# Optimization experiments

Hardware: AMD Instinct MI355X
Metric: run time of the kernel (lower is better)

The kernel has to match this reference:

```python
import jax, jax.numpy as jnp
import numpy as np

WINDOW = 2  # window_size

def _causal_window_conv(x, W, b):
    # x: [B,T,D_in], W: [WINDOW, D_in, D_out], b: [D_out]
    # equivalent to left-padding x by WINDOW-1 zeros and a 'valid' conv
    B, T, _ = x.shape
    xp = jnp.pad(x, ((0, 0), (WINDOW - 1, 0), (0, 0)))  # [B, T+WINDOW-1, D_in]
    out = b
    for k in range(WINDOW):
        out = out + jnp.einsum('btd,de->bte', xp[:, k:k + T], W[k])
    return out  # [B,T,D_out]

def setup_inputs() -> dict:
    key = jax.random.key(0)
    ks = jax.random.split(key, 4)
    B, T, Din, Dout = 8, 4096, 256, 256
    scale = 0.05
    x = jax.random.normal(ks[0], (B, T, Din), dtype=jnp.float32)
    W_z = jax.random.normal(ks[1], (WINDOW, Din, Dout), dtype=jnp.float32) * scale
    W_f = jax.random.normal(ks[2], (WINDOW, Din, Dout), dtype=jnp.float32) * scale
    W_o = jax.random.normal(ks[3], (WINDOW, Din, Dout), dtype=jnp.float32) * scale
    b_z = jnp.zeros((Dout,), dtype=jnp.float32)
    b_f = jnp.zeros((Dout,), dtype=jnp.float32)
    b_o = jnp.zeros((Dout,), dtype=jnp.float32)
    return {"x": x, "W_z": W_z, "W_f": W_f, "W_o": W_o,
            "b_z": b_z, "b_f": b_f, "b_o": b_o}

def reference(x, W_z, W_f, W_o, b_z, b_f, b_o):
    # QRNN with fo-pooling (Bradbury et al. 2016), return_sequences=True
    z = jnp.tanh(_causal_window_conv(x, W_z, b_z))          # [B,T,D]
    f = jax.nn.sigmoid(_causal_window_conv(x, W_f, b_f))    # [B,T,D]
    o = jax.nn.sigmoid(_causal_window_conv(x, W_o, b_o))    # [B,T,D]

    def step(c, zfo):
        z_t, f_t, o_t = zfo
        c = f_t * c + (1.0 - f_t) * z_t   # fo-pooling recurrence
        h = o_t * c
        return c, h

    c0 = jnp.zeros(z.shape[::2], dtype=z.dtype)  # [B,D]
    # time-major for scan
    zfo = (z.transpose(1, 0, 2), f.transpose(1, 0, 2), o.transpose(1, 0, 2))
    _, hs = jax.lax.scan(step, c0, zfo)
    return hs.transpose(1, 0, 2)  # [B,T,D]
```

## Files before the change

kernel.cpp:

```cpp
#include <hip/hip_runtime.h>
#include <hip/hip_bf16.h>
#include <hip/hip_fp16.h>

#define BDIM 8
#define TDIM 4096
#define DDIM 256
#define MDIM (BDIM * TDIM)
#define NCHUNK 256
#define LCHUNK (TDIM / NCHUNK)

typedef _Float16 f16x8 __attribute__((ext_vector_type(8)));
typedef _Float16 f16x4 __attribute__((ext_vector_type(4)));
typedef float f32x4 __attribute__((ext_vector_type(4)));

__device__ __forceinline__ float sigmoid_(float x) {
    return 1.0f / (1.0f + __expf(-x));
}
__device__ __forceinline__ float tanh_(float x) {
    return 2.0f / (1.0f + __expf(-2.0f * x)) - 1.0f;
}

#define GLOAD_LDS16(g, l)                                                    \
    __builtin_amdgcn_global_load_lds(                                        \
        (const __attribute__((address_space(1))) void*)(g),                  \
        (__attribute__((address_space(3))) void*)(l), 16, 0, 0)

__global__ __launch_bounds__(256) void convert_x(const float* __restrict__ x,
                                                 _Float16* __restrict__ xpad) {
    const int tp = blockIdx.x * 4 + (threadIdx.x >> 6);
    const int b = blockIdx.y;
    const int q = threadIdx.x & 63;
    if (tp > TDIM) return;
    float4 v = make_float4(0.f, 0.f, 0.f, 0.f);
    if (tp > 0)
        v = *(const float4*)(x + ((size_t)b * TDIM + tp - 1) * DDIM + q * 4);
    f16x4 h;
    h[0] = (_Float16)v.x; h[1] = (_Float16)v.y;
    h[2] = (_Float16)v.z; h[3] = (_Float16)v.w;
    *(f16x4*)(xpad + ((size_t)b * (TDIM + 1) + tp) * DDIM + q * 4) = h;
}

__global__ __launch_bounds__(256) void convert_w(
    const float* __restrict__ Wz, const float* __restrict__ Wf,
    const float* __restrict__ Wo, _Float16* __restrict__ Wt) {
    const int idx = blockIdx.x * 256 + threadIdx.x;
    const int n = idx & 255;
    const int kin = (idx >> 8) & 255;
    const int w = (idx >> 16) & 1;
    const int g = idx >> 17;
    const float* W = (g == 0) ? Wz : (g == 1) ? Wf : Wo;
    const float v = W[(size_t)w * 65536 + (size_t)kin * 256 + n];
    Wt[((size_t)g * 256 + n) * 512 + w * 256 + kin] = (_Float16)v;
}

__global__ __launch_bounds__(256) void gates_mfma(
    const _Float16* __restrict__ xpad, const _Float16* __restrict__ Wt,
    const float* __restrict__ bz, const float* __restrict__ bfv,
    const float* __restrict__ bo,
    _Float16* __restrict__ zbuf, _Float16* __restrict__ fbuf,
    _Float16* __restrict__ obuf) {
    const int hw = blockIdx.x;
    const int logical = (hw & 7) * 192 + (hw >> 3);
    const int mblk = logical / 6;
    const int rem = logical - mblk * 6;
    const int gate = rem % 3;
    const int nblk = rem / 3;
    const int m0 = mblk * 128;
    const int n0 = nblk * 128;

    const int tid = threadIdx.x;
    const int lane = tid & 63;
    const int wave = tid >> 6;
    const int wr = wave >> 1;
    const int wc = wave & 1;

    __shared__ __align__(16) char smem[65536];

    const int s = wave * 64 + lane;
    const int r1 = s >> 2;
    const int kc = (((s & 3) ^ ((s >> 3) & 3))) * 8;

    const int b = m0 >> 12;
    const int t0 = m0 & (TDIM - 1);

    const _Float16* srcA1 =
        xpad + ((size_t)b * (TDIM + 1) + t0 + r1) * DDIM + kc;
    const _Float16* srcA2 = srcA1 + (size_t)64 * DDIM;
    const _Float16* srcB1 = Wt + ((size_t)gate * 256 + n0 + r1) * 512 + kc;
    const _Float16* srcB2 = srcB1 + (size_t)64 * 512;

#define STAGE_(slot, t)                                                      \
    {                                                                        \
        char* dA = smem + (slot) * 16384 + wave * 1024;                      \
        char* dB = smem + (slot) * 16384 + 8192 + wave * 1024;               \
        GLOAD_LDS16(srcA1 + (t) * 32, dA);                                   \
        GLOAD_LDS16(srcA2 + (t) * 32, dA + 4096);                            \
        GLOAD_LDS16(srcB1 + (t) * 32, dB);                                   \
        GLOAD_LDS16(srcB2 + (t) * 32, dB + 4096);                            \
    }

    f32x4 acc[4][4] = {};
    const int am = lane & 15;
    const int kswz = (((lane >> 4) ^ ((lane >> 1) & 3))) * 8;

    STAGE_(0, 0);
    STAGE_(1, 1);
    STAGE_(2, 2);

#pragma unroll
    for (int it = 0; it < 16; ++it) {
        if (it <= 13)
            asm volatile("s_waitcnt vmcnt(8)" ::: "memory");
        else if (it == 14)
            asm volatile("s_waitcnt vmcnt(4)" ::: "memory");
        else
            asm volatile("s_waitcnt vmcnt(0)" ::: "memory");
        __builtin_amdgcn_s_barrier();
        __builtin_amdgcn_sched_barrier(0);
        if (it < 13) STAGE_((it + 3) & 3, it + 3);
        __builtin_amdgcn_sched_barrier(0);

        const _Float16* Ab = (const _Float16*)(smem + (it & 3) * 16384);
        const _Float16* Bb = (const _Float16*)(smem + (it & 3) * 16384 + 8192);

        f16x8 a[4], bb[4];
#pragma unroll
        for (int i = 0; i < 4; ++i)
            a[i] = *(const f16x8*)(Ab + (wr * 64 + i * 16 + am) * 32 + kswz);
#pragma unroll
        for (int j = 0; j < 4; ++j)
            bb[j] = *(const f16x8*)(Bb + (wc * 64 + j * 16 + am) * 32 + kswz);

        asm volatile("s_waitcnt lgkmcnt(0)" ::: "memory");
        __builtin_amdgcn_sched_barrier(0);
        __builtin_amdgcn_s_setprio(1);
#pragma unroll
        for (int i = 0; i < 4; ++i)
#pragma unroll
            for (int j = 0; j < 4; ++j)
                acc[i][j] = __builtin_amdgcn_mfma_f32_16x16x32_f16(
                    bb[j], a[i], acc[i][j], 0, 0, 0);
        __builtin_amdgcn_s_setprio(0);
        __builtin_amdgcn_sched_barrier(0);
    }
#undef STAGE_

    const float* bias = (gate == 0) ? bz : (gate == 1) ? bfv : bo;
    _Float16* outp = (gate == 0) ? zbuf : (gate == 1) ? fbuf : obuf;
    const int nq = (lane >> 4) * 4;
#pragma unroll
    for (int i = 0; i < 4; ++i) {
        const size_t gm = (size_t)(m0 + wr * 64 + i * 16 + am);
#pragma unroll
        for (int j = 0; j < 4; ++j) {
            const int gc = n0 + wc * 64 + j * 16 + nq;
            const float4 b4 = *(const float4*)(bias + gc);
            f32x4 v = acc[i][j];
            f16x4 h;
            if (gate == 0) {
                h[0] = (_Float16)tanh_(v[0] + b4.x);
                h[1] = (_Float16)tanh_(v[1] + b4.y);
                h[2] = (_Float16)tanh_(v[2] + b4.z);
                h[3] = (_Float16)tanh_(v[3] + b4.w);
            } else {
                h[0] = (_Float16)sigmoid_(v[0] + b4.x);
                h[1] = (_Float16)sigmoid_(v[1] + b4.y);
                h[2] = (_Float16)sigmoid_(v[2] + b4.z);
                h[3] = (_Float16)sigmoid_(v[3] + b4.w);
            }
            *(f16x4*)(outp + gm * DDIM + gc) = h;
        }
    }
}

__global__ __launch_bounds__(256) void scan_pass1(
    const _Float16* __restrict__ zbuf, const _Float16* __restrict__ fbuf,
    float* __restrict__ aggA, float* __restrict__ aggB) {
    const int idx = blockIdx.x * 256 + threadIdx.x;
    const int d4 = idx & 63;
    const int chunk = (idx >> 6) & (NCHUNK - 1);
    const int b = idx >> 14;

    const size_t row0 = (size_t)b * TDIM + (size_t)chunk * LCHUNK;
    const int2* zp = (const int2*)zbuf + row0 * 64 + d4;
    const int2* fp = (const int2*)fbuf + row0 * 64 + d4;

    float A[4], c[4];
#pragma unroll
    for (int e = 0; e < 4; ++e) { A[e] = 1.0f; c[e] = 0.0f; }

    for (int i = 0; i < LCHUNK; ++i) {
        int2 fv = *fp;
        int2 zv = *zp;
        const _Float16* fh = (const _Float16*)&fv;
        const _Float16* zh = (const _Float16*)&zv;
#pragma unroll
        for (int e = 0; e < 4; ++e) {
            const float f = (float)fh[e];
            const float z = (float)zh[e];
            A[e] *= f;
            c[e] = f * c[e] + (1.0f - f) * z;
        }
        fp += 64;
        zp += 64;
    }
    ((float4*)aggA)[idx] = make_float4(A[0], A[1], A[2], A[3]);
    ((float4*)aggB)[idx] = make_float4(c[0], c[1], c[2], c[3]);
}

__global__ __launch_bounds__(256) void carry_scan(
    const float* __restrict__ aggA, const float* __restrict__ aggB,
    float* __restrict__ carry) {
    const int g = blockIdx.x * 256 + threadIdx.x;
    const int d = g & 255;
    const int b = g >> 8;
    const size_t base = (size_t)b * NCHUNK * 256 + d;

    float c = 0.0f;
    for (int ch0 = 0; ch0 < NCHUNK; ch0 += 16) {
        float A[16], Bv[16];
#pragma unroll
        for (int u = 0; u < 16; ++u) {
            const size_t p = base + (size_t)(ch0 + u) * 256;
            A[u] = aggA[p];
            Bv[u] = aggB[p];
        }
#pragma unroll
        for (int u = 0; u < 16; ++u) {
            const size_t p = base + (size_t)(ch0 + u) * 256;
            carry[p] = c;
            c = A[u] * c + Bv[u];
        }
    }
}

__global__ __launch_bounds__(256) void scan_pass2(
    const _Float16* __restrict__ zbuf, const _Float16* __restrict__ fbuf,
    const _Float16* __restrict__ obuf, const float* __restrict__ carry,
    float* __restrict__ out) {
    const int idx = blockIdx.x * 256 + threadIdx.x;
    const int d4 = idx & 63;
    const int chunk = (idx >> 6) & (NCHUNK - 1);
    const int b = idx >> 14;

    float c[4];
    const float4 c0 = ((const float4*)carry)[idx];
    c[0] = c0.x; c[1] = c0.y; c[2] = c0.z; c[3] = c0.w;

    const size_t row0 = (size_t)b * TDIM + (size_t)chunk * LCHUNK;
    const int2* zp = (const int2*)zbuf + row0 * 64 + d4;
    const int2* fp = (const int2*)fbuf + row0 * 64 + d4;
    const int2* op = (const int2*)obuf + row0 * 64 + d4;
    float4* hp = (float4*)out + row0 * 64 + d4;

    for (int i = 0; i < LCHUNK; ++i) {
        int2 fv = *fp;
        int2 zv = *zp;
        int2 ov = *op;
        const _Float16* fh = (const _Float16*)&fv;
        const _Float16* zh = (const _Float16*)&zv;
        const _Float16* oh = (const _Float16*)&ov;
        float h[4];
#pragma unroll
        for (int e = 0; e < 4; ++e) {
            const float f = (float)fh[e];
            const float z = (float)zh[e];
            c[e] = f * c[e] + (1.0f - f) * z;
            h[e] = (float)oh[e] * c[e];
        }
        *hp = make_float4(h[0], h[1], h[2], h[3]);
        fp += 64;
        zp += 64;
        op += 64;
        hp += 64;
    }
}

extern "C" void kernel_launch(void* const* d_in, const int* in_sizes, int n_in,
                              void* d_out, int out_size, void* d_ws,
                              size_t ws_size, hipStream_t stream) {
    const float* x = (const float*)d_in[0];
    const float* Wz = (const float*)d_in[1];
    const float* Wf = (const float*)d_in[2];
    const float* Wo = (const float*)d_in[3];
    const float* bz = (const float*)d_in[4];
    const float* bfv = (const float*)d_in[5];
    const float* bo = (const float*)d_in[6];
    float* out = (float*)d_out;

    char* p = (char*)d_ws;
    _Float16* xpad = (_Float16*)p;  p += (size_t)BDIM * (TDIM + 1) * DDIM * 2;
    _Float16* Wt = (_Float16*)p;    p += (size_t)3 * 256 * 512 * 2;
    _Float16* zbuf = (_Float16*)p;  p += (size_t)MDIM * DDIM * 2;
    _Float16* fbuf = (_Float16*)p;  p += (size_t)MDIM * DDIM * 2;
    _Float16* obuf = (_Float16*)p;  p += (size_t)MDIM * DDIM * 2;
    float* aggA = (float*)p;        p += (size_t)BDIM * NCHUNK * DDIM * 4;
    float* aggB = (float*)p;        p += (size_t)BDIM * NCHUNK * DDIM * 4;
    float* carry = (float*)p;

    convert_x<<<dim3((TDIM + 4) / 4, BDIM), 256, 0, stream>>>(x, xpad);
    convert_w<<<(3 * 2 * 256 * 256) / 256, 256, 0, stream>>>(Wz, Wf, Wo, Wt);

    gates_mfma<<<MDIM / 128 * (DDIM / 128) * 3, 256, 0, stream>>>(
        xpad, Wt, bz, bfv, bo, zbuf, fbuf, obuf);

    scan_pass1<<<(BDIM * NCHUNK * 64) / 256, 256, 0, stream>>>(zbuf, fbuf,
                                                               aggA, aggB);
    carry_scan<<<(BDIM * DDIM) / 256, 256, 0, stream>>>(aggA, aggB, carry);
    scan_pass2<<<(BDIM * NCHUNK * 64) / 256, 256, 0, stream>>>(zbuf, fbuf,
                                                               obuf, carry, out);
}
```

Before: 166.3 us.

## Merge prep kernels and double-buffer LDS fragment reads in gate GEMM

Fuses the x and W conversion kernels into one launch to cut a kernel launch. In the MFMA GEMM loop, the LDS-to-register fragment reads for the next k-step now go into a second register buffer and are issued before the current step's MFMAs. The waitcnt schedule is reworked so the LDS reads overlap the matrix math. This costs more VGPRs for the doubled fragments, and the relaxed waitcnts must remain correct.

```diff
diff --git a/kernel.cpp b/kernel.cpp
--- a/kernel.cpp
+++ b/kernel.cpp
@@ -25,10 +25,26 @@
         (const __attribute__((address_space(1))) void*)(g),                  \
         (__attribute__((address_space(3))) void*)(l), 16, 0, 0)
 
-__global__ __launch_bounds__(256) void convert_x(const float* __restrict__ x,
-                                                 _Float16* __restrict__ xpad) {
-    const int tp = blockIdx.x * 4 + (threadIdx.x >> 6);
-    const int b = blockIdx.y;
+__global__ __launch_bounds__(256) void prep(
+    const float* __restrict__ x, _Float16* __restrict__ xpad,
+    const float* __restrict__ Wz, const float* __restrict__ Wf,
+    const float* __restrict__ Wo, _Float16* __restrict__ Wt) {
+    const int bx = blockIdx.x;
+    if (bx < 1536) {
+        const int idx = bx * 256 + threadIdx.x;
+        const int n = idx & 255;
+        const int kin = (idx >> 8) & 255;
+        const int w = (idx >> 16) & 1;
+        const int g = idx >> 17;
+        const float* W = (g == 0) ? Wz : (g == 1) ? Wf : Wo;
+        const float v = W[(size_t)w * 65536 + (size_t)kin * 256 + n];
+        Wt[((size_t)g * 256 + n) * 512 + w * 256 + kin] = (_Float16)v;
+        return;
+    }
+    const int bxx = bx - 1536;
+    const int b = bxx / 1025;
+    const int tb = bxx - b * 1025;
+    const int tp = tb * 4 + (threadIdx.x >> 6);
     const int q = threadIdx.x & 63;
     if (tp > TDIM) return;
     float4 v = make_float4(0.f, 0.f, 0.f, 0.f);
@@ -38,19 +54,6 @@
     h[0] = (_Float16)v.x; h[1] = (_Float16)v.y;
     h[2] = (_Float16)v.z; h[3] = (_Float16)v.w;
     *(f16x4*)(xpad + ((size_t)b * (TDIM + 1) + tp) * DDIM + q * 4) = h;
-}
-
-__global__ __launch_bounds__(256) void convert_w(
-    const float* __restrict__ Wz, const float* __restrict__ Wf,
-    const float* __restrict__ Wo, _Float16* __restrict__ Wt) {
-    const int idx = blockIdx.x * 256 + threadIdx.x;
-    const int n = idx & 255;
-    const int kin = (idx >> 8) & 255;
-    const int w = (idx >> 16) & 1;
-    const int g = idx >> 17;
-    const float* W = (g == 0) ? Wz : (g == 1) ? Wf : Wo;
-    const float v = W[(size_t)w * 65536 + (size_t)kin * 256 + n];
-    Wt[((size_t)g * 256 + n) * 512 + w * 256 + kin] = (_Float16)v;
 }
 
 __global__ __launch_bounds__(256) void gates_mfma(
@@ -100,38 +103,45 @@
     }
 
     f32x4 acc[4][4] = {};
+    f16x8 aR[2][4], bR[2][4];
     const int am = lane & 15;
     const int kswz = (((lane >> 4) ^ ((lane >> 1) & 3))) * 8;
+
+#define READ_FRAGS(buf, slot)                                                \
+    {                                                                        \
+        const _Float16* Ab = (const _Float16*)(smem + (slot) * 16384);       \
+        const _Float16* Bb =                                                 \
+            (const _Float16*)(smem + (slot) * 16384 + 8192);                 \
+        _Pragma("unroll") for (int i = 0; i < 4; ++i) aR[buf][i] =           \
+            *(const f16x8*)(Ab + (wr * 64 + i * 16 + am) * 32 + kswz);       \
+        _Pragma("unroll") for (int j = 0; j < 4; ++j) bR[buf][j] =           \
+            *(const f16x8*)(Bb + (wc * 64 + j * 16 + am) * 32 + kswz);       \
+    }
 
     STAGE_(0, 0);
     STAGE_(1, 1);
     STAGE_(2, 2);
-
-#pragma unroll
-    for (int it = 0; it < 16; ++it) {
-        if (it <= 13)
-            asm volatile("s_waitcnt vmcnt(8)" ::: "memory");
-        else if (it == 14)
-            asm volatile("s_waitcnt vmcnt(4)" ::: "memory");
-        else
-            asm volatile("s_waitcnt vmcnt(0)" ::: "memory");
-        __builtin_amdgcn_s_barrier();
-        __builtin_amdgcn_sched_barrier(0);
-        if (it < 13) STAGE_((it + 3) & 3, it + 3);
-        __builtin_amdgcn_sched_barrier(0);
-
-        const _Float16* Ab = (const _Float16*)(smem + (it & 3) * 16384);
-        const _Float16* Bb = (const _Float16*)(smem + (it & 3) * 16384 + 8192);
-
-        f16x8 a[4], bb[4];
-#pragma unroll
-        for (int i = 0; i < 4; ++i)
-            a[i] = *(const f16x8*)(Ab + (wr * 64 + i * 16 + am) * 32 + kswz);
-#pragma unroll
-        for (int j = 0; j < 4; ++j)
-            bb[j] = *(const f16x8*)(Bb + (wc * 64 + j * 16 + am) * 32 + kswz);
-
-        asm volatile("s_waitcnt lgkmcnt(0)" ::: "memory");
+    asm volatile("s_waitcnt vmcnt(8)" ::: "memory");
+    __builtin_amdgcn_s_barrier();
+    __builtin_amdgcn_sched_barrier(0);
+    READ_FRAGS(0, 0);
+
+#pragma unroll
+    for (int t = 0; t < 16; ++t) {
+        const int cur = t & 1;
+        if (t < 15) {
+            if (t <= 13)
+                asm volatile("s_waitcnt vmcnt(4)" ::: "memory");
+            else
+                asm volatile("s_waitcnt vmcnt(0)" ::: "memory");
+            __builtin_amdgcn_s_barrier();
+            __builtin_amdgcn_sched_barrier(0);
+            if (t < 13) STAGE_((t + 3) & 3, t + 3);
+            READ_FRAGS(cur ^ 1, (t + 1) & 3);
+            asm volatile("s_waitcnt lgkmcnt(8)" ::: "memory");
+        } else {
+            asm volatile("s_waitcnt lgkmcnt(0)" ::: "memory");
+        }
         __builtin_amdgcn_sched_barrier(0);
         __builtin_amdgcn_s_setprio(1);
 #pragma unroll
@@ -139,11 +149,11 @@
 #pragma unroll
             for (int j = 0; j < 4; ++j)
                 acc[i][j] = __builtin_amdgcn_mfma_f32_16x16x32_f16(
-                    bb[j], a[i], acc[i][j], 0, 0, 0);
+                    bR[cur][j], aR[cur][i], acc[i][j], 0, 0, 0);
         __builtin_amdgcn_s_setprio(0);
-        __builtin_amdgcn_sched_barrier(0);
     }
 #undef STAGE_
+#undef READ_FRAGS
 
     const float* bias = (gate == 0) ? bz : (gate == 1) ? bfv : bo;
     _Float16* outp = (gate == 0) ? zbuf : (gate == 1) ? fbuf : obuf;
@@ -298,8 +308,7 @@
     float* aggB = (float*)p;        p += (size_t)BDIM * NCHUNK * DDIM * 4;
     float* carry = (float*)p;
 
-    convert_x<<<dim3((TDIM + 4) / 4, BDIM), 256, 0, stream>>>(x, xpad);
-    convert_w<<<(3 * 2 * 256 * 256) / 256, 256, 0, stream>>>(Wz, Wf, Wo, Wt);
+    prep<<<1536 + 1025 * BDIM, 256, 0, stream>>>(x, xpad, Wz, Wf, Wo, Wt);
 
     gates_mfma<<<MDIM / 128 * (DDIM / 128) * 3, 256, 0, stream>>>(
         xpad, Wt, bz, bfv, bo, zbuf, fbuf, obuf);
```

Result: no change. 164.8 us (-0.9%).

## Merge conversion kernels and switch GEMM to double-buffered LDS for occupancy

Applied to the files above, without the earlier changes.

Fuses the x and weight fp16 conversion kernels into one launch, removing a kernel launch. The gates GEMM drops from a 4-stage LDS pipeline (64KB) to a 2-stage double buffer (32KB) with launch_bounds requesting 4 blocks per CU. Higher occupancy is meant to hide global-load latency across blocks instead of within one block, at the cost of waiting on vmcnt(0) every iteration, which gives less prefetch depth per block.

```diff
diff --git a/kernel.cpp b/kernel.cpp
--- a/kernel.cpp
+++ b/kernel.cpp
@@ -25,10 +25,26 @@
         (const __attribute__((address_space(1))) void*)(g),                  \
         (__attribute__((address_space(3))) void*)(l), 16, 0, 0)
 
-__global__ __launch_bounds__(256) void convert_x(const float* __restrict__ x,
-                                                 _Float16* __restrict__ xpad) {
-    const int tp = blockIdx.x * 4 + (threadIdx.x >> 6);
-    const int b = blockIdx.y;
+__global__ __launch_bounds__(256) void prep(
+    const float* __restrict__ x, _Float16* __restrict__ xpad,
+    const float* __restrict__ Wz, const float* __restrict__ Wf,
+    const float* __restrict__ Wo, _Float16* __restrict__ Wt) {
+    const int bx = blockIdx.x;
+    if (bx < 1536) {
+        const int idx = bx * 256 + threadIdx.x;
+        const int n = idx & 255;
+        const int kin = (idx >> 8) & 255;
+        const int w = (idx >> 16) & 1;
+        const int g = idx >> 17;
+        const float* W = (g == 0) ? Wz : (g == 1) ? Wf : Wo;
+        const float v = W[(size_t)w * 65536 + (size_t)kin * 256 + n];
+        Wt[((size_t)g * 256 + n) * 512 + w * 256 + kin] = (_Float16)v;
+        return;
+    }
+    const int bxx = bx - 1536;
+    const int b = bxx / 1025;
+    const int tb = bxx - b * 1025;
+    const int tp = tb * 4 + (threadIdx.x >> 6);
     const int q = threadIdx.x & 63;
     if (tp > TDIM) return;
     float4 v = make_float4(0.f, 0.f, 0.f, 0.f);
@@ -40,20 +56,7 @@
     *(f16x4*)(xpad + ((size_t)b * (TDIM + 1) + tp) * DDIM + q * 4) = h;
 }
 
-__global__ __launch_bounds__(256) void convert_w(
-    const float* __restrict__ Wz, const float* __restrict__ Wf,
-    const float* __restrict__ Wo, _Float16* __restrict__ Wt) {
-    const int idx = blockIdx.x * 256 + threadIdx.x;
-    const int n = idx & 255;
-    const int kin = (idx >> 8) & 255;
-    const int w = (idx >> 16) & 1;
-    const int g = idx >> 17;
-    const float* W = (g == 0) ? Wz : (g == 1) ? Wf : Wo;
-    const float v = W[(size_t)w * 65536 + (size_t)kin * 256 + n];
-    Wt[((size_t)g * 256 + n) * 512 + w * 256 + kin] = (_Float16)v;
-}
-
-__global__ __launch_bounds__(256) void gates_mfma(
+__global__ __launch_bounds__(256, 4) void gates_mfma(
     const _Float16* __restrict__ xpad, const _Float16* __restrict__ Wt,
     const float* __restrict__ bz, const float* __restrict__ bfv,
     const float* __restrict__ bo,
@@ -74,7 +77,7 @@
     const int wr = wave >> 1;
     const int wc = wave & 1;
 
-    __shared__ __align__(16) char smem[65536];
+    __shared__ __align__(16) char smem[32768];
 
     const int s = wave * 64 + lane;
     const int r1 = s >> 2;
@@ -104,24 +107,16 @@
     const int kswz = (((lane >> 4) ^ ((lane >> 1) & 3))) * 8;
 
     STAGE_(0, 0);
-    STAGE_(1, 1);
-    STAGE_(2, 2);
-
-#pragma unroll
-    for (int it = 0; it < 16; ++it) {
-        if (it <= 13)
-            asm volatile("s_waitcnt vmcnt(8)" ::: "memory");
-        else if (it == 14)
-            asm volatile("s_waitcnt vmcnt(4)" ::: "memory");
-        else
-            asm volatile("s_waitcnt vmcnt(0)" ::: "memory");
+
+#pragma unroll
+    for (int t = 0; t < 16; ++t) {
+        asm volatile("s_waitcnt vmcnt(0)" ::: "memory");
         __builtin_amdgcn_s_barrier();
         __builtin_amdgcn_sched_barrier(0);
-        if (it < 13) STAGE_((it + 3) & 3, it + 3);
-        __builtin_amdgcn_sched_barrier(0);
-
-        const _Float16* Ab = (const _Float16*)(smem + (it & 3) * 16384);
-        const _Float16* Bb = (const _Float16*)(smem + (it & 3) * 16384 + 8192);
+        if (t < 15) STAGE_((t + 1) & 1, t + 1);
+
+        const _Float16* Ab = (const _Float16*)(smem + (t & 1) * 16384);
+        const _Float16* Bb = (const _Float16*)(smem + (t & 1) * 16384 + 8192);
 
         f16x8 a[4], bb[4];
 #pragma unroll
@@ -141,7 +136,6 @@
                 acc[i][j] = __builtin_amdgcn_mfma_f32_16x16x32_f16(
                     bb[j], a[i], acc[i][j], 0, 0, 0);
         __builtin_amdgcn_s_setprio(0);
-        __builtin_amdgcn_sched_barrier(0);
     }
 #undef STAGE_
 
@@ -298,8 +292,7 @@
     float* aggB = (float*)p;        p += (size_t)BDIM * NCHUNK * DDIM * 4;
     float* carry = (float*)p;
 
-    convert_x<<<dim3((TDIM + 4) / 4, BDIM), 256, 0, stream>>>(x, xpad);
-    convert_w<<<(3 * 2 * 256 * 256) / 256, 256, 0, stream>>>(Wz, Wf, Wo, Wt);
+    prep<<<1536 + 1025 * BDIM, 256, 0, stream>>>(x, xpad, Wz, Wf, Wo, Wt);
 
     gates_mfma<<<MDIM / 128 * (DDIM / 128) * 3, 256, 0, stream>>>(
         xpad, Wt, bz, bfv, bo, zbuf, fbuf, obuf);
```

New measurement: 162.7 us. 2.2% less time.
